# Optimization experiments

Hardware: AMD Instinct MI355X
Metric: run time of the kernel (lower is better)

Reference implementation:

```python
import jax, jax.numpy as jnp
import numpy as np
from jax import lax

V, Dm, NL, N, K, E = 32000, 1024, 4, 16, 4, 2
Di = Dm * E
B, T = 1, 2048
EPS = 1e-5


def setup_inputs() -> dict:
    key = jax.random.key(0)
    ks = jax.random.split(key, 8)
    s = 0.02
    A_init = jnp.log(jnp.arange(1.0, N + 1, dtype=jnp.float32))  # (N,)
    return {
        "idx": jax.random.randint(ks[0], (B, T), 0, V),
        "emb": jax.random.normal(ks[1], (V, Dm), dtype=jnp.float32) * s,
        "norm_w": jnp.ones((NL, Dm), jnp.float32),
        "in_proj_w": jax.random.normal(ks[2], (NL, 2 * Di, Dm), dtype=jnp.float32) * s,
        "conv_w": jax.random.normal(ks[3], (NL, Di, 1, K), dtype=jnp.float32) * s,
        "conv_b": jnp.zeros((NL, Di), jnp.float32),
        "x_proj_w": jax.random.normal(ks[4], (NL, 2 * N + 1, Di), dtype=jnp.float32) * s,
        "dt_proj_w": jax.random.normal(ks[5], (NL, Di, 1), dtype=jnp.float32) * s,
        "dt_proj_b": jnp.zeros((NL, Di), jnp.float32),
        "A_log": jnp.broadcast_to(A_init[None, None, :], (NL, Di, N)).copy(),
        "D_param": jnp.ones((NL, Di), jnp.float32),
        "out_proj_w": jax.random.normal(ks[6], (NL, Dm, Di), dtype=jnp.float32) * s,
        "norm_f_w": jnp.ones((Dm,), jnp.float32),
    }


def _rmsnorm(x, w):
    rms = jnp.sqrt(jnp.mean(x * x, axis=-1, keepdims=True) + EPS)
    return x / rms * w


def _mamba_block(x, in_w, cw, cb, xp_w, dt_w, dt_b, A_log, Dp, out_w):
    # x: (B, L, Dm)
    xz = x @ in_w.T                       # (B, L, 2*Di)
    x_ssm, z = xz[..., :Di], xz[..., Di:]
    # causal depthwise conv (torch pads both sides then crops -> left-pad only)
    xc = x_ssm.transpose(0, 2, 1)         # (B, Di, L)
    xc = lax.conv_general_dilated(
        xc, cw, window_strides=(1,), padding=[(K - 1, 0)],
        dimension_numbers=("NCH", "OIH", "NCH"), feature_group_count=Di)
    xc = xc + cb[None, :, None]
    u = jax.nn.silu(xc.transpose(0, 2, 1))  # (B, L, Di)
    # selective SSM
    A = -jnp.exp(A_log)                     # (Di, N)
    xp = u @ xp_w.T                         # (B, L, 2N+1)
    dt_raw, Bv, Cv = xp[..., :1], xp[..., 1:1 + N], xp[..., 1 + N:]
    dt = jax.nn.softplus(dt_raw * dt_w[:, 0] + dt_b)  # (B, L, Di)

    def step(h, inp):
        dt_t, Bv_t, Cv_t, u_t = inp          # (B,Di),(B,N),(B,N),(B,Di)
        dA = jnp.exp(dt_t[..., None] * A)    # (B, Di, N)
        h = dA * h + (dt_t * u_t)[..., None] * Bv_t[:, None, :]
        y_t = jnp.einsum("bdn,bn->bd", h, Cv_t)
        return h, y_t

    h0 = jnp.zeros((x.shape[0], Di, N), u.dtype)
    xs = (dt.transpose(1, 0, 2), Bv.transpose(1, 0, 2),
          Cv.transpose(1, 0, 2), u.transpose(1, 0, 2))
    _, ys = lax.scan(step, h0, xs)           # (L, B, Di)
    y = ys.transpose(1, 0, 2) + u * Dp
    y = y * jax.nn.silu(z)
    return y @ out_w.T


def reference(idx, emb, norm_w, in_proj_w, conv_w, conv_b, x_proj_w,
              dt_proj_w, dt_proj_b, A_log, D_param, out_proj_w, norm_f_w):
    x = emb[idx]                             # (B, T, Dm); dropout=0 in eval
    for l in range(NL):
        x = x + _mamba_block(_rmsnorm(x, norm_w[l]), in_proj_w[l], conv_w[l],
                             conv_b[l], x_proj_w[l], dt_proj_w[l], dt_proj_b[l],
                             A_log[l], D_param[l], out_proj_w[l])
    x = _rmsnorm(x, norm_f_w)
    logits = x @ emb.T                       # tied lm_head
    return logits
```

## Files before the change

kernel.cpp:

```cpp
#include <hip/hip_runtime.h>
#include <hip/hip_bf16.h>

typedef __hip_bfloat16 bf16;
typedef __attribute__((ext_vector_type(8))) short short8;
typedef __attribute__((ext_vector_type(4))) float f32x4;

#define TT 2048
#define DM 1024
#define DI 2048
#define NLAYER 4
#define NST 16
#define KC 4
#define VOCAB 32000
#define XPS 33
#define NCHUNK 64
#define CLEN 32

__device__ __forceinline__ float us2f(unsigned short u) {
    union { float f; unsigned int i; } c; c.i = ((unsigned int)u) << 16; return c.f;
}
__device__ __forceinline__ float ldin(const void* p, size_t i, int f32) {
    return f32 ? ((const float*)p)[i] : us2f(((const unsigned short*)p)[i]);
}
__device__ __forceinline__ unsigned short f2us(float f) {
    bf16 h = __float2bfloat16(f);
    return *(unsigned short*)&h;
}
__device__ __forceinline__ size_t hidx(int n, int c, int d) {
    return ((size_t)n * NCHUNK + c) * DI + d;
}

__global__ void detect_kernel(const unsigned int* __restrict__ w_bits, int* __restrict__ flag) {
    if (threadIdx.x == 0) *flag = (w_bits[0] == 0x3F800000u) ? 1 : 0;
}

__global__ void cvt8_dual_kernel(const float* __restrict__ sA, unsigned short* __restrict__ dA, int n8A,
                                 const float* __restrict__ sB, unsigned short* __restrict__ dB, int n8B) {
    int i = blockIdx.x * 256 + threadIdx.x;
    const float* s; unsigned short* d;
    if (i < n8A) { s = sA; d = dA; }
    else { i -= n8A; if (i >= n8B) return; s = sB; d = dB; }
    float4 a = ((const float4*)s)[2 * i];
    float4 b = ((const float4*)s)[2 * i + 1];
    unsigned int w0 = (unsigned int)f2us(a.x) | ((unsigned int)f2us(a.y) << 16);
    unsigned int w1 = (unsigned int)f2us(a.z) | ((unsigned int)f2us(a.w) << 16);
    unsigned int w2 = (unsigned int)f2us(b.x) | ((unsigned int)f2us(b.y) << 16);
    unsigned int w3 = (unsigned int)f2us(b.z) | ((unsigned int)f2us(b.w) << 16);
    ((uint4*)d)[i] = make_uint4(w0, w1, w2, w3);
}

__global__ void embed_kernel(const int* __restrict__ idx, const void* __restrict__ emb,
                             float* __restrict__ x, const int* __restrict__ fl) {
    int f32 = *fl;
    int t = blockIdx.x, q = threadIdx.x;
    size_t src = (size_t)idx[t] * DM + q * 4;
    float4 v;
    if (f32) v = *(const float4*)((const float*)emb + src);
    else {
        ushort4 h = *(const ushort4*)((const unsigned short*)emb + src);
        v = make_float4(us2f(h.x), us2f(h.y), us2f(h.z), us2f(h.w));
    }
    ((float4*)x)[(size_t)t * (DM / 4) + q] = v;
}

__global__ void rmsnorm_kernel(const float* __restrict__ x, const void* __restrict__ w,
                               size_t wofs, bf16* __restrict__ ob, const int* __restrict__ fl) {
    int f32 = *fl;
    int t = blockIdx.x, tid = threadIdx.x;
    int wv = tid >> 6, lane = tid & 63;
    float4 v = ((const float4*)(x + (size_t)t * DM))[tid];
    float s = v.x * v.x + v.y * v.y + v.z * v.z + v.w * v.w;
#pragma unroll
    for (int o = 1; o < 64; o <<= 1) s += __shfl_xor(s, o, 64);
    __shared__ float red[4];
    if (lane == 0) red[wv] = s;
    __syncthreads();
    float inv = rsqrtf((red[0] + red[1] + red[2] + red[3]) / (float)DM + 1e-5f);
    float w0, w1, w2, w3;
    if (f32) {
        float4 wq = ((const float4*)((const float*)w + wofs))[tid];
        w0 = wq.x; w1 = wq.y; w2 = wq.z; w3 = wq.w;
    } else {
        ushort4 wq = ((const ushort4*)((const unsigned short*)w + wofs))[tid];
        w0 = us2f(wq.x); w1 = us2f(wq.y); w2 = us2f(wq.z); w3 = us2f(wq.w);
    }
    uint2 o;
    o.x = (unsigned int)f2us(v.x * inv * w0) | ((unsigned int)f2us(v.y * inv * w1) << 16);
    o.y = (unsigned int)f2us(v.z * inv * w2) | ((unsigned int)f2us(v.w * inv * w3) << 16);
    ((uint2*)(ob + (size_t)t * DM))[tid] = o;
}

template<int BM>
__global__ __launch_bounds__(256, 2)
void gemm_mfma(const bf16* __restrict__ A16, const bf16* __restrict__ B16,
               const float* __restrict__ Res, float* __restrict__ Cf, bf16* __restrict__ C16,
               int MT, int NT, int Kk) {
    constexpr int MR = BM / 32;
    constexpr int AQ = BM / 64;
    int Nn = NT << 7;
    __shared__ __align__(16) unsigned short As[BM * 32];
    __shared__ __align__(16) unsigned short Bs[128 * 32];
    int tid = threadIdx.x;
    int w = tid >> 6, lane = tid & 63;
    int h = lane >> 4, r = lane & 15;

    int nwg = MT * NT;
    int bid = blockIdx.x;
    int swz = ((nwg & 7) == 0) ? ((bid & 7) * (nwg >> 3) + (bid >> 3)) : bid;
    int mt = swz % MT, nt = swz / MT;
    int m0 = mt * BM, n0 = nt << 7;

    const unsigned short* Ap = (const unsigned short*)A16;
    const unsigned short* Bp = (const unsigned short*)B16;

    int skof = (lane & 3) << 3;
    int srowA = w * (BM / 4) + (lane >> 2);
    int srowB = (w << 5) + (lane >> 2);
    const unsigned short* gA = Ap + (size_t)(m0 + srowA) * Kk + skof;
    const unsigned short* gB = Bp + (size_t)(n0 + srowB) * Kk + skof;
    unsigned short* lA = As + ((w * (BM / 4)) << 5);
    unsigned short* lB = Bs + (w << 10);

    f32x4 acc[MR][4];
#pragma unroll
    for (int i = 0; i < MR; i++)
#pragma unroll
        for (int j = 0; j < 4; j++) acc[i][j] = (f32x4){0.f, 0.f, 0.f, 0.f};

    int wr = w >> 1, wc = w & 1;
    const unsigned short* rA = As + (((wr * (BM / 2)) + r) << 5) + (h << 3);
    const unsigned short* rB = Bs + (((wc << 6) + r) << 5) + (h << 3);

    for (int k0 = 0; k0 < Kk; k0 += 32) {
#pragma unroll
        for (int q = 0; q < AQ; q++)
            __builtin_amdgcn_global_load_lds(
                (const __attribute__((address_space(1))) void*)(gA + k0 + (size_t)(q * 16) * Kk),
                (__attribute__((address_space(3))) void*)(lA + q * 512), 16, 0, 0);
#pragma unroll
        for (int q = 0; q < 2; q++)
            __builtin_amdgcn_global_load_lds(
                (const __attribute__((address_space(1))) void*)(gB + k0 + (size_t)(q * 16) * Kk),
                (__attribute__((address_space(3))) void*)(lB + q * 512), 16, 0, 0);
        __syncthreads();
        short8 af[MR], bfr[4];
#pragma unroll
        for (int mi = 0; mi < MR; mi++) af[mi] = *(const short8*)(rA + (mi << 9));
#pragma unroll
        for (int ni = 0; ni < 4; ni++) bfr[ni] = *(const short8*)(rB + (ni << 9));
#pragma unroll
        for (int mi = 0; mi < MR; mi++)
#pragma unroll
            for (int ni = 0; ni < 4; ni++)
                acc[mi][ni] = __builtin_amdgcn_mfma_f32_16x16x32_bf16(
                    af[mi], bfr[ni], acc[mi][ni], 0, 0, 0);
        __syncthreads();
    }
#pragma unroll
    for (int mi = 0; mi < MR; mi++) {
#pragma unroll
        for (int j = 0; j < 4; j++) {
            int row = m0 + wr * (BM / 2) + (mi << 4) + (h << 2) + j;
            size_t base = (size_t)row * Nn + n0 + (wc << 6) + r;
#pragma unroll
            for (int ni = 0; ni < 4; ni++) {
                float v = acc[mi][ni][j];
                size_t o = base + (ni << 4);
                if (Res) v += Res[o];
                if (Cf)  Cf[o] = v;
                if (C16) C16[o] = __float2bfloat16(v);
            }
        }
    }
}

__global__ void cxp_kernel(const float* __restrict__ xz,
                           const void* __restrict__ cw, size_t cwofs,
                           const void* __restrict__ cb, size_t cbofs,
                           const void* __restrict__ xpw, size_t xpwofs,
                           float* __restrict__ u, float* __restrict__ xp,
                           const int* __restrict__ fl) {
    int f32 = *fl;
    int t = blockIdx.x, tid = threadIdx.x;
    int wv = tid >> 6, lane = tid & 63;
    int d0 = tid * 8;
    float uv[8];
#pragma unroll
    for (int k = 0; k < 8; k++) uv[k] = ldin(cb, cbofs + d0 + k, f32);
#pragma unroll
    for (int j = 0; j < KC; j++) {
        int tt = t - (KC - 1) + j;
        if (tt < 0) continue;
        const float* row = xz + (size_t)tt * (2 * DI) + d0;
        float4 v0 = *(const float4*)row;
        float4 v1 = *(const float4*)(row + 4);
        float vv[8] = {v0.x, v0.y, v0.z, v0.w, v1.x, v1.y, v1.z, v1.w};
#pragma unroll
        for (int k = 0; k < 8; k++)
            uv[k] += ldin(cw, cwofs + (size_t)(d0 + k) * KC + j, f32) * vv[k];
    }
#pragma unroll
    for (int k = 0; k < 8; k++) { float s = uv[k]; uv[k] = s / (1.f + __expf(-s)); }
    float* ur = u + (size_t)t * DI + d0;
    *(float4*)ur       = make_float4(uv[0], uv[1], uv[2], uv[3]);
    *(float4*)(ur + 4) = make_float4(uv[4], uv[5], uv[6], uv[7]);

    float p[XPS];
    if (f32) {
        const float* wb = (const float*)xpw + xpwofs + d0;
#pragma unroll
        for (int n = 0; n < XPS; n++) {
            const float* wp = wb + (size_t)n * DI;
            float4 w0 = *(const float4*)wp, w1 = *(const float4*)(wp + 4);
            p[n] = uv[0] * w0.x + uv[1] * w0.y + uv[2] * w0.z + uv[3] * w0.w
                 + uv[4] * w1.x + uv[5] * w1.y + uv[6] * w1.z + uv[7] * w1.w;
        }
    } else {
        const unsigned short* wb = (const unsigned short*)xpw + xpwofs + d0;
#pragma unroll
        for (int n = 0; n < XPS; n++) {
            uint4 wq = *(const uint4*)(wb + (size_t)n * DI);
            p[n] = uv[0] * us2f(wq.x & 0xffff) + uv[1] * us2f(wq.x >> 16)
                 + uv[2] * us2f(wq.y & 0xffff) + uv[3] * us2f(wq.y >> 16)
                 + uv[4] * us2f(wq.z & 0xffff) + uv[5] * us2f(wq.z >> 16)
                 + uv[6] * us2f(wq.w & 0xffff) + uv[7] * us2f(wq.w >> 16);
        }
    }
    __shared__ float red[4 * XPS];
#pragma unroll
    for (int n = 0; n < XPS; n++) {
        float v = p[n];
#pragma unroll
        for (int s_ = 1; s_ < 64; s_ <<= 1) v += __shfl_xor(v, s_, 64);
        if (lane == 0) red[wv * XPS + n] = v;
    }
    __syncthreads();
    if (tid < XPS)
        xp[t * XPS + tid] = red[tid] + red[XPS + tid] + red[2 * XPS + tid] + red[3 * XPS + tid];
}

__global__ void scanA_kernel(const float* __restrict__ xp, const float* __restrict__ u,
                             const void* __restrict__ dtw, size_t dtwofs,
                             const void* __restrict__ dtb, size_t dtbofs,
                             const void* __restrict__ A_log, size_t aofs,
                             float* __restrict__ S, float* __restrict__ hend,
                             const int* __restrict__ fl) {
    int f32 = *fl;
    int c = blockIdx.y;
    int d = blockIdx.x * 256 + threadIdx.x;
    __shared__ float xps[CLEN * XPS];
    for (int i = threadIdx.x; i < CLEN * XPS; i += 256) xps[i] = xp[c * CLEN * XPS + i];
    __syncthreads();
    float dw = ldin(dtw, dtwofs + d, f32);
    float db = ldin(dtb, dtbofs + d, f32);
    float Ar[NST], hh[NST];
#pragma unroll
    for (int n = 0; n < NST; n++) {
        Ar[n] = -expf(ldin(A_log, aofs + (size_t)d * NST + n, f32));
        hh[n] = 0.f;
    }
    float ssum = 0.f;
    const float* urow = u + (size_t)c * CLEN * DI + d;
    for (int tt = 0; tt < CLEN; tt++) {
        float s = xps[tt * XPS] * dw + db;
        float dtv = (s > 20.f) ? s : log1pf(__expf(s));
        float uvv = urow[(size_t)tt * DI];
        float du = dtv * uvv;
        ssum += dtv;
        const float* bb = &xps[tt * XPS + 1];
#pragma unroll
        for (int n = 0; n < NST; n++)
            hh[n] = __expf(dtv * Ar[n]) * hh[n] + du * bb[n];
    }
    S[c * DI + d] = ssum;
#pragma unroll
    for (int n = 0; n < NST; n++) hend[hidx(n, c, d)] = hh[n];
}

__global__ void scanB_kernel(const float* __restrict__ S, float* __restrict__ hend,
                             const void* __restrict__ A_log, size_t aofs,
                             const int* __restrict__ fl) {
    int f32 = *fl;
    int i = blockIdx.x * 256 + threadIdx.x;
    int d = i & (DI - 1), n = i >> 11;
    float A = -expf(ldin(A_log, aofs + (size_t)d * NST + n, f32));
    float H = 0.f;
    for (int c = 0; c < NCHUNK; c++) {
        size_t o = hidx(n, c, d);
        float he = hend[o];
        hend[o] = H;
        H = __expf(A * S[c * DI + d]) * H + he;
    }
}

__global__ void scanC_kernel(const float* __restrict__ xp, const float* __restrict__ u,
                             const float* __restrict__ xz,
                             const void* __restrict__ dtw, size_t dtwofs,
                             const void* __restrict__ dtb, size_t dtbofs,
                             const void* __restrict__ A_log, size_t aofs,
                             const void* __restrict__ Dp, size_t dofs,
                             const float* __restrict__ hcar, bf16* __restrict__ y16,
                             const int* __restrict__ fl) {
    int f32 = *fl;
    int c = blockIdx.y;
    int d = blockIdx.x * 256 + threadIdx.x;
    __shared__ float xps[CLEN * XPS];
    for (int i = threadIdx.x; i < CLEN * XPS; i += 256) xps[i] = xp[c * CLEN * XPS + i];
    __syncthreads();
    float dw = ldin(dtw, dtwofs + d, f32);
    float db = ldin(dtb, dtbofs + d, f32);
    float Dpv = ldin(Dp, dofs + d, f32);
    float Ar[NST], hh[NST];
#pragma unroll
    for (int n = 0; n < NST; n++) {
        Ar[n] = -expf(ldin(A_log, aofs + (size_t)d * NST + n, f32));
        hh[n] = hcar[hidx(n, c, d)];
    }
    for (int tt = 0; tt < CLEN; tt++) {
        int t = c * CLEN + tt;
        float s = xps[tt * XPS] * dw + db;
        float dtv = (s > 20.f) ? s : log1pf(__expf(s));
        float uvv = u[(size_t)t * DI + d];
        float du = dtv * uvv;
        const float* bb = &xps[tt * XPS + 1];
        const float* cc = &xps[tt * XPS + 1 + NST];
        float accv = 0.f;
#pragma unroll
        for (int n = 0; n < NST; n++) {
            hh[n] = __expf(dtv * Ar[n]) * hh[n] + du * bb[n];
            accv += hh[n] * cc[n];
        }
        float z = xz[(size_t)t * (2 * DI) + DI + d];
        float sz = z / (1.f + __expf(-z));
        y16[(size_t)t * DI + d] = __float2bfloat16((accv + uvv * Dpv) * sz);
    }
}

extern "C" void kernel_launch(void* const* d_in, const int* in_sizes, int n_in,
                              void* d_out, int out_size, void* d_ws, size_t ws_size,
                              hipStream_t stream) {
    const int*  idx       = (const int*)d_in[0];
    const void* emb       = d_in[1];
    const void* norm_w    = d_in[2];
    const void* in_proj_w = d_in[3];
    const void* conv_w    = d_in[4];
    const void* conv_b    = d_in[5];
    const void* x_proj_w  = d_in[6];
    const void* dt_proj_w = d_in[7];
    const void* dt_proj_b = d_in[8];
    const void* A_log     = d_in[9];
    const void* D_param   = d_in[10];
    const void* out_proj_w= d_in[11];
    const void* norm_f_w  = d_in[12];

    float* ws   = (float*)d_ws;
    float* xz   = ws;
    float* u    = ws + 8388608;
    float* hend = ws + 12582912;
    bf16*  W16A = (bf16*)(ws + 14680064);
    bf16*  W16B = (bf16*)(ws + 16777216);
    float* S    = ws + 17825792;
    float* xp   = ws + 17956864;
    float* x    = ws + 18024448;
    bf16*  xn16 = (bf16*)(ws + 20121600);
    bf16*  y16  = (bf16*)(ws + 21170176);
    int*   fl   = (int*)(ws + 23267328);
    bf16*  emb16= (bf16*)ws;

    long long esz = in_sizes ? (long long)in_sizes[1] : -1;
    int isf32 = (esz == (long long)VOCAB * DM * 2) ? 0 : 1;

    detect_kernel<<<1, 64, 0, stream>>>((const unsigned int*)norm_w, fl);
    embed_kernel<<<TT, 256, 0, stream>>>(idx, emb, x, fl);

    for (int l = 0; l < NLAYER; l++) {
        const bf16* Bin;
        const bf16* Bout;
        if (isf32) {
            int n8A = 2 * DI * DM / 8, n8B = DM * DI / 8;
            cvt8_dual_kernel<<<(n8A + n8B + 255) / 256, 256, 0, stream>>>(
                (const float*)in_proj_w + (size_t)l * 2 * DI * DM, (unsigned short*)W16A, n8A,
                (const float*)out_proj_w + (size_t)l * DM * DI, (unsigned short*)W16B, n8B);
            Bin = W16A; Bout = W16B;
        } else {
            Bin  = (const bf16*)in_proj_w  + (size_t)l * 2 * DI * DM;
            Bout = (const bf16*)out_proj_w + (size_t)l * DM * DI;
        }

        rmsnorm_kernel<<<TT, 256, 0, stream>>>(x, norm_w, (size_t)l * DM, xn16, fl);
        gemm_mfma<128><<<(TT / 128) * (2 * DI / 128), 256, 0, stream>>>(
            xn16, Bin, nullptr, xz, nullptr, TT / 128, 2 * DI / 128, DM);
        cxp_kernel<<<TT, 256, 0, stream>>>(
            xz, conv_w, (size_t)l * DI * KC, conv_b, (size_t)l * DI,
            x_proj_w, (size_t)l * XPS * DI, u, xp, fl);
        scanA_kernel<<<dim3(DI / 256, NCHUNK), 256, 0, stream>>>(
            xp, u, dt_proj_w, (size_t)l * DI, dt_proj_b, (size_t)l * DI,
            A_log, (size_t)l * DI * NST, S, hend, fl);
        scanB_kernel<<<DI * NST / 256, 256, 0, stream>>>(
            S, hend, A_log, (size_t)l * DI * NST, fl);
        scanC_kernel<<<dim3(DI / 256, NCHUNK), 256, 0, stream>>>(
            xp, u, xz, dt_proj_w, (size_t)l * DI, dt_proj_b, (size_t)l * DI,
            A_log, (size_t)l * DI * NST, D_param, (size_t)l * DI, hend, y16, fl);
        gemm_mfma<64><<<(TT / 64) * (DM / 128), 256, 0, stream>>>(
            y16, Bout, x, x, nullptr, TT / 64, DM / 128, DI);
    }

    rmsnorm_kernel<<<TT, 256, 0, stream>>>(x, norm_f_w, 0, xn16, fl);

    const bf16* Bemb;
    if (isf32) {
        int n8 = VOCAB * DM / 8;
        cvt8_dual_kernel<<<(n8 + 255) / 256, 256, 0, stream>>>(
            (const float*)emb, (unsigned short*)emb16, n8, nullptr, nullptr, 0);
        Bemb = emb16;
    } else {
        Bemb = (const bf16*)emb;
    }
    if (isf32)
        gemm_mfma<128><<<(TT / 128) * (VOCAB / 128), 256, 0, stream>>>(
            xn16, Bemb, nullptr, (float*)d_out, nullptr, TT / 128, VOCAB / 128, DM);
    else
        gemm_mfma<128><<<(TT / 128) * (VOCAB / 128), 256, 0, stream>>>(
            xn16, Bemb, nullptr, nullptr, (bf16*)d_out, TT / 128, VOCAB / 128, DM);
}
```

Baseline: 1.554 ms.

## Deepen GEMM K-tile to 64, stage epilogue through LDS, shrink M tiles

Raises the GEMM K-step from 32 to 64 so each barrier pair covers two MFMA k-substeps, which halves the loop and sync count. The epilogue now stages accumulators through shared memory and writes float4/packed-bf16 rows for coalesced global stores and residual reads. The in_proj and out_proj GEMMs use smaller M tiles (64 and 32) to launch more workgroups. The costs are more LDS per block, which may lower occupancy, and smaller tiles give less operand reuse. LDS rows are unpadded at 64 elements, which risks bank conflicts on the fragment reads.

```diff
diff --git a/kernel.cpp b/kernel.cpp
--- a/kernel.cpp
+++ b/kernel.cpp
@@ -95,11 +95,15 @@
 void gemm_mfma(const bf16* __restrict__ A16, const bf16* __restrict__ B16,
                const float* __restrict__ Res, float* __restrict__ Cf, bf16* __restrict__ C16,
                int MT, int NT, int Kk) {
+    constexpr int BK = 64;
     constexpr int MR = BM / 32;
-    constexpr int AQ = BM / 64;
+    constexpr int AQ = BM / 32;
     int Nn = NT << 7;
-    __shared__ __align__(16) unsigned short As[BM * 32];
-    __shared__ __align__(16) unsigned short Bs[128 * 32];
+    __shared__ __align__(16) char smem[(BM + 128) * BK * 2];
+    unsigned short* As = (unsigned short*)smem;
+    unsigned short* Bs = As + BM * BK;
+    float* Cs = (float*)smem;
+
     int tid = threadIdx.x;
     int w = tid >> 6, lane = tid & 63;
     int h = lane >> 4, r = lane & 15;
@@ -113,13 +117,10 @@
     const unsigned short* Ap = (const unsigned short*)A16;
     const unsigned short* Bp = (const unsigned short*)B16;
 
-    int skof = (lane & 3) << 3;
-    int srowA = w * (BM / 4) + (lane >> 2);
-    int srowB = (w << 5) + (lane >> 2);
-    const unsigned short* gA = Ap + (size_t)(m0 + srowA) * Kk + skof;
-    const unsigned short* gB = Bp + (size_t)(n0 + srowB) * Kk + skof;
-    unsigned short* lA = As + ((w * (BM / 4)) << 5);
-    unsigned short* lB = Bs + (w << 10);
+    int srow = tid >> 3;
+    int skof = (tid & 7) << 3;
+    const unsigned short* gA = Ap + (size_t)(m0 + srow) * Kk + skof;
+    const unsigned short* gB = Bp + (size_t)(n0 + srow) * Kk + skof;
 
     f32x4 acc[MR][4];
 #pragma unroll
@@ -128,49 +129,73 @@
         for (int j = 0; j < 4; j++) acc[i][j] = (f32x4){0.f, 0.f, 0.f, 0.f};
 
     int wr = w >> 1, wc = w & 1;
-    const unsigned short* rA = As + (((wr * (BM / 2)) + r) << 5) + (h << 3);
-    const unsigned short* rB = Bs + (((wc << 6) + r) << 5) + (h << 3);
-
-    for (int k0 = 0; k0 < Kk; k0 += 32) {
+    const unsigned short* rA = As + (((wr * (BM / 2)) + r) << 6) + (h << 3);
+    const unsigned short* rB = Bs + (((wc << 6) + r) << 6) + (h << 3);
+
+    for (int k0 = 0; k0 < Kk; k0 += BK) {
 #pragma unroll
         for (int q = 0; q < AQ; q++)
             __builtin_amdgcn_global_load_lds(
-                (const __attribute__((address_space(1))) void*)(gA + k0 + (size_t)(q * 16) * Kk),
-                (__attribute__((address_space(3))) void*)(lA + q * 512), 16, 0, 0);
-#pragma unroll
-        for (int q = 0; q < 2; q++)
+                (const __attribute__((address_space(1))) void*)(gA + k0 + (size_t)(q * 32) * Kk),
+                (__attribute__((address_space(3))) void*)(As + q * 2048 + (w << 9)), 16, 0, 0);
+#pragma unroll
+        for (int q = 0; q < 4; q++)
             __builtin_amdgcn_global_load_lds(
-                (const __attribute__((address_space(1))) void*)(gB + k0 + (size_t)(q * 16) * Kk),
-                (__attribute__((address_space(3))) void*)(lB + q * 512), 16, 0, 0);
+                (const __attribute__((address_space(1))) void*)(gB + k0 + (size_t)(q * 32) * Kk),
+                (__attribute__((address_space(3))) void*)(Bs + q * 2048 + (w << 9)), 16, 0, 0);
         __syncthreads();
-        short8 af[MR], bfr[4];
-#pragma unroll
-        for (int mi = 0; mi < MR; mi++) af[mi] = *(const short8*)(rA + (mi << 9));
-#pragma unroll
-        for (int ni = 0; ni < 4; ni++) bfr[ni] = *(const short8*)(rB + (ni << 9));
-#pragma unroll
-        for (int mi = 0; mi < MR; mi++)
+#pragma unroll
+        for (int kk = 0; kk < 2; kk++) {
+            short8 af[MR], bfr[4];
+#pragma unroll
+            for (int mi = 0; mi < MR; mi++)
+                af[mi] = *(const short8*)(rA + (mi << 10) + (kk << 5));
 #pragma unroll
             for (int ni = 0; ni < 4; ni++)
-                acc[mi][ni] = __builtin_amdgcn_mfma_f32_16x16x32_bf16(
-                    af[mi], bfr[ni], acc[mi][ni], 0, 0, 0);
+                bfr[ni] = *(const short8*)(rB + (ni << 10) + (kk << 5));
+#pragma unroll
+            for (int mi = 0; mi < MR; mi++)
+#pragma unroll
+                for (int ni = 0; ni < 4; ni++)
+                    acc[mi][ni] = __builtin_amdgcn_mfma_f32_16x16x32_bf16(
+                        af[mi], bfr[ni], acc[mi][ni], 0, 0, 0);
+        }
         __syncthreads();
     }
 #pragma unroll
-    for (int mi = 0; mi < MR; mi++) {
-#pragma unroll
-        for (int j = 0; j < 4; j++) {
-            int row = m0 + wr * (BM / 2) + (mi << 4) + (h << 2) + j;
-            size_t base = (size_t)row * Nn + n0 + (wc << 6) + r;
-#pragma unroll
-            for (int ni = 0; ni < 4; ni++) {
-                float v = acc[mi][ni][j];
-                size_t o = base + (ni << 4);
-                if (Res) v += Res[o];
-                if (Cf)  Cf[o] = v;
-                if (C16) C16[o] = __float2bfloat16(v);
+    for (int p = 0; p < BM / 32; p++) {
+#pragma unroll
+        for (int mi = 0; mi < MR; mi++) {
+            int mloc = wr * (BM / 2) + mi * 16;
+            if ((mloc >> 5) != p) continue;
+            int lr0 = (mloc & 31) + (h << 2);
+#pragma unroll
+            for (int j = 0; j < 4; j++)
+#pragma unroll
+                for (int ni = 0; ni < 4; ni++)
+                    Cs[(lr0 + j) * 132 + (wc << 6) + (ni << 4) + r] = acc[mi][ni][j];
+        }
+        __syncthreads();
+#pragma unroll
+        for (int q2 = 0; q2 < 4; q2++) {
+            int f = q2 * 256 + tid;
+            int rr = f >> 5, c4 = f & 31;
+            int grow = m0 + p * 32 + rr;
+            size_t go = (size_t)grow * Nn + n0 + (c4 << 2);
+            float4 v = *(const float4*)&Cs[rr * 132 + (c4 << 2)];
+            if (Res) {
+                float4 rv = *(const float4*)(Res + go);
+                v.x += rv.x; v.y += rv.y; v.z += rv.z; v.w += rv.w;
             }
-        }
+            if (Cf) *(float4*)(Cf + go) = v;
+            if (C16) {
+                uint2 o;
+                o.x = (unsigned int)f2us(v.x) | ((unsigned int)f2us(v.y) << 16);
+                o.y = (unsigned int)f2us(v.z) | ((unsigned int)f2us(v.w) << 16);
+                *(uint2*)((unsigned short*)C16 + go) = o;
+            }
+        }
+        __syncthreads();
     }
 }
 
@@ -388,8 +413,8 @@
         }
 
         rmsnorm_kernel<<<TT, 256, 0, stream>>>(x, norm_w, (size_t)l * DM, xn16, fl);
-        gemm_mfma<128><<<(TT / 128) * (2 * DI / 128), 256, 0, stream>>>(
-            xn16, Bin, nullptr, xz, nullptr, TT / 128, 2 * DI / 128, DM);
+        gemm_mfma<64><<<(TT / 64) * (2 * DI / 128), 256, 0, stream>>>(
+            xn16, Bin, nullptr, xz, nullptr, TT / 64, 2 * DI / 128, DM);
         cxp_kernel<<<TT, 256, 0, stream>>>(
             xz, conv_w, (size_t)l * DI * KC, conv_b, (size_t)l * DI,
             x_proj_w, (size_t)l * XPS * DI, u, xp, fl);
@@ -401,8 +426,8 @@
         scanC_kernel<<<dim3(DI / 256, NCHUNK), 256, 0, stream>>>(
             xp, u, xz, dt_proj_w, (size_t)l * DI, dt_proj_b, (size_t)l * DI,
             A_log, (size_t)l * DI * NST, D_param, (size_t)l * DI, hend, y16, fl);
-        gemm_mfma<64><<<(TT / 64) * (DM / 128), 256, 0, stream>>>(
-            y16, Bout, x, x, nullptr, TT / 64, DM / 128, DI);
+        gemm_mfma<32><<<(TT / 32) * (DM / 128), 256, 0, stream>>>(
+            y16, Bout, x, x, nullptr, TT / 32, DM / 128, DI);
     }
 
     rmsnorm_kernel<<<TT, 256, 0, stream>>>(x, norm_f_w, 0, xn16, fl);
```

Measured after the change: 1.553 ms. No clear change (-0.1%).
